# Kernel tuning notes

Hardware: AMD Instinct MI355X
Metric: run time of the kernel (lower is better)

## Reference

```python
import jax, jax.numpy as jnp
import numpy as np

B, D, U = 256, 2048, 2048  # batch, input_dim, units
EPS = 1e-8


def setup_inputs() -> dict:
    key = jax.random.key(0)
    ks = jax.random.split(key, 20)
    sd = 1.0 / np.sqrt(D)
    su = 1.0 / np.sqrt(U)
    inp = {
        'x': jax.random.normal(ks[0], (B, D), jnp.float32),
        'h_prev': jax.random.normal(ks[1], (B, U), jnp.float32),
        'c_prev': jax.random.normal(ks[2], (B, U), jnp.float32),
        'n_prev': jax.random.uniform(ks[3], (B, U), jnp.float32),
        'm_prev': jax.random.normal(ks[4], (B, U), jnp.float32),
        # input-to-gate weights (Dense with bias), keras layout [in, out]
        'Wz': jax.random.normal(ks[5], (D, U), jnp.float32) * sd,
        'Wi': jax.random.normal(ks[6], (D, U), jnp.float32) * sd,
        'Wf': jax.random.normal(ks[7], (D, U), jnp.float32) * sd,
        'Wo': jax.random.normal(ks[8], (D, U), jnp.float32) * sd,
        'bz': jnp.zeros((U,), jnp.float32),
        'bi': jnp.zeros((U,), jnp.float32),
        'bf': jnp.zeros((U,), jnp.float32),
        'bo': jnp.zeros((U,), jnp.float32),
        # recurrent weights (Dense without bias)
        'Uz': jax.random.normal(ks[9], (U, U), jnp.float32) * su,
        'Ui': jax.random.normal(ks[10], (U, U), jnp.float32) * su,
        'Uf': jax.random.normal(ks[11], (U, U), jnp.float32) * su,
        'Uo': jax.random.normal(ks[12], (U, U), jnp.float32) * su,
    }
    return inp


def reference(x, h_prev, c_prev, n_prev, m_prev,
              Wz, Wi, Wf, Wo, bz, bi, bf, bo, Uz, Ui, Uf, Uo):
    # fuse the 8 small GEMMs into 2 wide GEMMs (same math, gates split after)
    W = jnp.concatenate([Wz, Wi, Wf, Wo], axis=1)      # [D, 4U]
    Uc = jnp.concatenate([Uz, Ui, Uf, Uo], axis=1)     # [U, 4U]
    b = jnp.concatenate([bz, bi, bf, bo], axis=0)      # [4U]
    pre = x @ W + h_prev @ Uc + b                      # [B, 4U]
    z_tilde, i_tilde, f_tilde, o_tilde = jnp.split(pre, 4, axis=1)

    # exponential-gate stabilization (forget_gate_type='exponential')
    m_t = jnp.maximum(i_tilde + m_prev, i_tilde)
    i_t = jnp.exp(i_tilde - m_t)
    f_t = jnp.exp(f_tilde + m_prev - m_t)

    o_t = jax.nn.sigmoid(o_tilde)
    z_t = jnp.tanh(z_tilde)

    c_t = f_t * c_prev + i_t * z_t
    n_t = f_t * n_prev + i_t
    h_t = o_t * (c_t / (n_t + EPS))
    return jnp.stack([h_t, c_t, n_t, m_t], axis=0)  # [4, B, U]
```

## Files before the change

kernel.cpp:

```cpp
#include <hip/hip_runtime.h>
#include <cstdint>
#include <cstddef>

#define B_   256
#define D_   2048
#define U_   2048
#define NTOT 8192
#define BN   32
#define BK   64
#define KC   2048
#define ITERS (KC / BK)

typedef _Float16 half8 __attribute__((ext_vector_type(8)));
typedef float floatx16 __attribute__((ext_vector_type(16)));

__global__ __launch_bounds__(256) void prep_kernel(
    const float* __restrict__ x, const float* __restrict__ h,
    _Float16* __restrict__ Ahi)
{
    int gid   = blockIdx.x * 256 + threadIdx.x;
    int chunk = gid >> 8;
    int row   = gid & 255;
    int col0  = chunk * 8;
    const float* src = (col0 < D_) ? (x + row * D_ + col0)
                                   : (h + row * U_ + (col0 - D_));
    float4 v0 = *(const float4*)(src);
    float4 v1 = *(const float4*)(src + 4);
    float v[8] = {v0.x, v0.y, v0.z, v0.w, v1.x, v1.y, v1.z, v1.w};
    half8 hi;
#pragma unroll
    for (int i = 0; i < 8; ++i) hi[i] = (_Float16)v[i];
    *(half8*)(Ahi + (chunk * 256 + row) * 8) = hi;
}

__global__ __launch_bounds__(256) void gemm_kernel(
    const _Float16* __restrict__ Ahi,
    const float* __restrict__ Wz, const float* __restrict__ Wi,
    const float* __restrict__ Wf, const float* __restrict__ Wo,
    const float* __restrict__ Uz, const float* __restrict__ Ui,
    const float* __restrict__ Uf, const float* __restrict__ Uo,
    float* __restrict__ P)
{
    __shared__ __align__(16) _Float16 sA[2][8 * 256 * 8];
    __shared__ __align__(16) float    sB[2][BK * BN];

    const int t    = threadIdx.x;
    const int w    = t >> 6;
    const int lane = t & 63;
    const int lg   = lane >> 5;
    const int lm   = lane & 31;

    const int nblk = blockIdx.x;
    const int ks   = blockIdx.y;
    const int n0   = nblk * BN;
    const int g    = n0 >> 11;
    const int c0   = n0 & (U_ - 1);

    const float* wsel[8] = {Wz, Wi, Wf, Wo, Uz, Ui, Uf, Uo};
    const float* Bm = wsel[ks * 4 + g];
    const int chunk0 = ks * 256;

    const int arow_t = t;
    const int bk_t   = t >> 3;
    const int bc_t   = (t & 7) * 4;

    floatx16 acc[2] = {};

#define STAGE(kk, buf)                                                        \
    {                                                                         \
        int gch = chunk0 + (kk) * 8;                                          \
        _Pragma("unroll")                                                     \
        for (int i = 0; i < 8; ++i) {                                         \
            int gidx = ((gch + i) * 256 + arow_t) * 8;                        \
            int lidx = (i * 256 + arow_t) * 8;                                \
            __builtin_amdgcn_global_load_lds(                                 \
                (const __attribute__((address_space(1))) void*)(Ahi + gidx),  \
                (__attribute__((address_space(3))) void*)(&sA[buf][lidx]),    \
                16, 0, 0);                                                    \
        }                                                                     \
        _Pragma("unroll")                                                     \
        for (int j = 0; j < 2; ++j) {                                         \
            int krow = j * 32 + bk_t;                                         \
            const float* src = Bm + (size_t)((kk) * BK + krow) * U_ + c0 + bc_t; \
            __builtin_amdgcn_global_load_lds(                                 \
                (const __attribute__((address_space(1))) void*)(src),         \
                (__attribute__((address_space(3))) void*)(&sB[buf][krow * BN + bc_t]), \
                16, 0, 0);                                                    \
        }                                                                     \
    }

    STAGE(0, 0);
    __syncthreads();

    for (int kk = 0; kk < ITERS; ++kk) {
        int cur = kk & 1;
        if (kk + 1 < ITERS) STAGE(kk + 1, cur ^ 1);

#pragma unroll
        for (int kin = 0; kin < 4; ++kin) {
            half8 a0, a1, bf;
            {
                int chunkIdx = kin * 2 + lg;
                int row0 = w * 64 + lm;
                a0 = *(const half8*)(&sA[cur][(chunkIdx * 256 + row0) * 8]);
                a1 = *(const half8*)(&sA[cur][(chunkIdx * 256 + row0 + 32) * 8]);
            }
#pragma unroll
            for (int j = 0; j < 8; ++j) {
                float v = sB[cur][(kin * 16 + lg * 8 + j) * BN + lm];
                bf[j] = (_Float16)v;
            }
            acc[0] = __builtin_amdgcn_mfma_f32_32x32x16_f16(a0, bf, acc[0], 0, 0, 0);
            acc[1] = __builtin_amdgcn_mfma_f32_32x32x16_f16(a1, bf, acc[1], 0, 0, 0);
        }
        __syncthreads();
    }
#undef STAGE

    float* Pks = P + (size_t)ks * ((size_t)B_ * NTOT);
#pragma unroll
    for (int mt = 0; mt < 2; ++mt)
#pragma unroll
        for (int r = 0; r < 16; ++r) {
            int m = w * 64 + mt * 32 + 4 * lg + (r & 3) + 8 * (r >> 2);
            Pks[(size_t)m * NTOT + n0 + lm] = acc[mt][r];
        }
}

__global__ __launch_bounds__(256) void gates_kernel(
    const float* __restrict__ P,
    const float* __restrict__ c_prev, const float* __restrict__ n_prev,
    const float* __restrict__ m_prev,
    const float* __restrict__ bz, const float* __restrict__ bi,
    const float* __restrict__ bf, const float* __restrict__ bo,
    float* __restrict__ out)
{
    const size_t PS = (size_t)B_ * NTOT;
    const int OS = B_ * U_;
    int gid = blockIdx.x * 256 + threadIdx.x;
    int m = gid >> 9;
    int u = (gid & 511) * 4;

    float pre[4][4];
#pragma unroll
    for (int gi = 0; gi < 4; ++gi) {
        const float* base = P + (size_t)m * NTOT + gi * U_ + u;
        float4 s0 = *(const float4*)(base);
        float4 s1 = *(const float4*)(base + PS);
        pre[gi][0] = s0.x + s1.x;
        pre[gi][1] = s0.y + s1.y;
        pre[gi][2] = s0.z + s1.z;
        pre[gi][3] = s0.w + s1.w;
    }
    float4 bzv = *(const float4*)(bz + u);
    float4 biv = *(const float4*)(bi + u);
    float4 bfv = *(const float4*)(bf + u);
    float4 bov = *(const float4*)(bo + u);
    float bza[4] = {bzv.x, bzv.y, bzv.z, bzv.w};
    float bia[4] = {biv.x, biv.y, biv.z, biv.w};
    float bfa[4] = {bfv.x, bfv.y, bfv.z, bfv.w};
    float boa[4] = {bov.x, bov.y, bov.z, bov.w};

    float4 cp4 = *(const float4*)(c_prev + m * U_ + u);
    float4 np4 = *(const float4*)(n_prev + m * U_ + u);
    float4 mp4 = *(const float4*)(m_prev + m * U_ + u);
    float cpa[4] = {cp4.x, cp4.y, cp4.z, cp4.w};
    float npa[4] = {np4.x, np4.y, np4.z, np4.w};
    float mpa[4] = {mp4.x, mp4.y, mp4.z, mp4.w};

    float hr[4], cr[4], nr[4], mr[4];
#pragma unroll
    for (int e = 0; e < 4; ++e) {
        float zt = pre[0][e] + bza[e];
        float it = pre[1][e] + bia[e];
        float ft = pre[2][e] + bfa[e];
        float ot = pre[3][e] + boa[e];
        float mp = mpa[e];
        float m_t = fmaxf(it + mp, it);
        float i_t = expf(it - m_t);
        float f_t = expf(ft + mp - m_t);
        float o_t = 1.0f / (1.0f + expf(-ot));
        float z_t = tanhf(zt);
        float c_t = f_t * cpa[e] + i_t * z_t;
        float n_t = f_t * npa[e] + i_t;
        float h_t = o_t * (c_t / (n_t + 1e-8f));
        hr[e] = h_t; cr[e] = c_t; nr[e] = n_t; mr[e] = m_t;
    }
    float4 hv = {hr[0], hr[1], hr[2], hr[3]};
    float4 cv = {cr[0], cr[1], cr[2], cr[3]};
    float4 nv = {nr[0], nr[1], nr[2], nr[3]};
    float4 mv = {mr[0], mr[1], mr[2], mr[3]};
    *(float4*)(out + 0 * OS + m * U_ + u) = hv;
    *(float4*)(out + 1 * OS + m * U_ + u) = cv;
    *(float4*)(out + 2 * OS + m * U_ + u) = nv;
    *(float4*)(out + 3 * OS + m * U_ + u) = mv;
}

extern "C" void kernel_launch(void* const* d_in, const int* in_sizes, int n_in,
                              void* d_out, int out_size, void* d_ws, size_t ws_size,
                              hipStream_t stream)
{
    const float* x  = (const float*)d_in[0];
    const float* h  = (const float*)d_in[1];
    const float* cp = (const float*)d_in[2];
    const float* np = (const float*)d_in[3];
    const float* mp = (const float*)d_in[4];
    const float* Wz = (const float*)d_in[5];
    const float* Wi = (const float*)d_in[6];
    const float* Wf = (const float*)d_in[7];
    const float* Wo = (const float*)d_in[8];
    const float* bz = (const float*)d_in[9];
    const float* bi = (const float*)d_in[10];
    const float* bf = (const float*)d_in[11];
    const float* bo = (const float*)d_in[12];
    const float* Uz = (const float*)d_in[13];
    const float* Ui = (const float*)d_in[14];
    const float* Uf = (const float*)d_in[15];
    const float* Uo = (const float*)d_in[16];

    float* P = (float*)d_ws;
    _Float16* Ahi = (_Float16*)((char*)d_ws + (size_t)2 * B_ * NTOT * sizeof(float));

    prep_kernel<<<512, 256, 0, stream>>>(x, h, Ahi);
    gemm_kernel<<<dim3(256, 2), 256, 0, stream>>>(Ahi,
        Wz, Wi, Wf, Wo, Uz, Ui, Uf, Uo, P);
    gates_kernel<<<512, 256, 0, stream>>>(P, cp, np, mp, bz, bi, bf, bo,
        (float*)d_out);
}
```

Baseline: 210.7 us.

## Stream A operand from global, stage B as fp16 in padded LDS

```diff
diff --git a/kernel.cpp b/kernel.cpp
--- a/kernel.cpp
+++ b/kernel.cpp
@@ -2,14 +2,15 @@
 #include <cstdint>
 #include <cstddef>
 
-#define B_   256
-#define D_   2048
-#define U_   2048
-#define NTOT 8192
-#define BN   32
-#define BK   64
-#define KC   2048
-#define ITERS (KC / BK)
+#define B_    256
+#define D_    2048
+#define U_    2048
+#define NTOT  8192
+#define BN    32
+#define BK    128
+#define KSLICE 2048
+#define CHUNKS (KSLICE / BK)
+#define BPITCH 136
 
 typedef _Float16 half8 __attribute__((ext_vector_type(8)));
 typedef float floatx16 __attribute__((ext_vector_type(16)));
@@ -19,9 +20,9 @@
     _Float16* __restrict__ Ahi)
 {
     int gid   = blockIdx.x * 256 + threadIdx.x;
-    int chunk = gid >> 8;
+    int koct  = gid >> 8;
     int row   = gid & 255;
-    int col0  = chunk * 8;
+    int col0  = koct * 8;
     const float* src = (col0 < D_) ? (x + row * D_ + col0)
                                    : (h + row * U_ + (col0 - D_));
     float4 v0 = *(const float4*)(src);
@@ -30,7 +31,7 @@
     half8 hi;
 #pragma unroll
     for (int i = 0; i < 8; ++i) hi[i] = (_Float16)v[i];
-    *(half8*)(Ahi + (chunk * 256 + row) * 8) = hi;
+    *(half8*)(Ahi + (koct * 256 + row) * 8) = hi;
 }
 
 __global__ __launch_bounds__(256) void gemm_kernel(
@@ -41,8 +42,7 @@
     const float* __restrict__ Uf, const float* __restrict__ Uo,
     float* __restrict__ P)
 {
-    __shared__ __align__(16) _Float16 sA[2][8 * 256 * 8];
-    __shared__ __align__(16) float    sB[2][BK * BN];
+    __shared__ __align__(16) _Float16 sB[2][BN * BPITCH];
 
     const int t    = threadIdx.x;
     const int w    = t >> 6;
@@ -50,72 +50,68 @@
     const int lg   = lane >> 5;
     const int lm   = lane & 31;
 
-    const int nblk = blockIdx.x;
-    const int ks   = blockIdx.y;
-    const int n0   = nblk * BN;
-    const int g    = n0 >> 11;
-    const int c0   = n0 & (U_ - 1);
+    const int ntile = blockIdx.x;
+    const int ks    = blockIdx.y;
+    const int n0    = ntile * BN;
+    const int g     = n0 >> 11;
+    const int c0    = n0 & (U_ - 1);
+    const int koctB = ks * 256;
 
     const float* wsel[8] = {Wz, Wi, Wf, Wo, Uz, Ui, Uf, Uo};
-    const float* Bm = wsel[ks * 4 + g];
-    const int chunk0 = ks * 256;
-
-    const int arow_t = t;
-    const int bk_t   = t >> 3;
-    const int bc_t   = (t & 7) * 4;
+    const float* Bm   = wsel[ks * 4 + g];
+    const float* Bcol = Bm + c0 + lm;
+
+    const int bko = w * 2 + lg;
 
     floatx16 acc[2] = {};
-
-#define STAGE(kk, buf)                                                        \
+    float breg[2][8];
+
+#define LOAD_B(kk)                                                            \
     {                                                                         \
-        int gch = chunk0 + (kk) * 8;                                          \
-        _Pragma("unroll")                                                     \
-        for (int i = 0; i < 8; ++i) {                                         \
-            int gidx = ((gch + i) * 256 + arow_t) * 8;                        \
-            int lidx = (i * 256 + arow_t) * 8;                                \
-            __builtin_amdgcn_global_load_lds(                                 \
-                (const __attribute__((address_space(1))) void*)(Ahi + gidx),  \
-                (__attribute__((address_space(3))) void*)(&sA[buf][lidx]),    \
-                16, 0, 0);                                                    \
-        }                                                                     \
         _Pragma("unroll")                                                     \
         for (int j = 0; j < 2; ++j) {                                         \
-            int krow = j * 32 + bk_t;                                         \
-            const float* src = Bm + (size_t)((kk) * BK + krow) * U_ + c0 + bc_t; \
-            __builtin_amdgcn_global_load_lds(                                 \
-                (const __attribute__((address_space(1))) void*)(src),         \
-                (__attribute__((address_space(3))) void*)(&sB[buf][krow * BN + bc_t]), \
-                16, 0, 0);                                                    \
+            const float* src = Bcol + (size_t)((kk) * BK + (bko + 8 * j) * 8) * U_; \
+            _Pragma("unroll")                                                 \
+            for (int i = 0; i < 8; ++i)                                       \
+                breg[j][i] = src[(size_t)i * U_];                             \
         }                                                                     \
     }
 
-    STAGE(0, 0);
+#define WRITE_B(buf)                                                          \
+    {                                                                         \
+        _Pragma("unroll")                                                     \
+        for (int j = 0; j < 2; ++j) {                                         \
+            half8 hb;                                                         \
+            _Pragma("unroll")                                                 \
+            for (int i = 0; i < 8; ++i) hb[i] = (_Float16)breg[j][i];         \
+            *(half8*)(&sB[buf][lm * BPITCH + (bko + 8 * j) * 8]) = hb;        \
+        }                                                                     \
+    }
+
+    LOAD_B(0);
+    WRITE_B(0);
     __syncthreads();
 
-    for (int kk = 0; kk < ITERS; ++kk) {
+    const int arow0 = w * 64 + lm;
+
+    for (int kk = 0; kk < CHUNKS; ++kk) {
         int cur = kk & 1;
-        if (kk + 1 < ITERS) STAGE(kk + 1, cur ^ 1);
-
-#pragma unroll
-        for (int kin = 0; kin < 4; ++kin) {
-            half8 a0, a1, bf;
-            {
-                int chunkIdx = kin * 2 + lg;
-                int row0 = w * 64 + lm;
-                a0 = *(const half8*)(&sA[cur][(chunkIdx * 256 + row0) * 8]);
-                a1 = *(const half8*)(&sA[cur][(chunkIdx * 256 + row0 + 32) * 8]);
-            }
-#pragma unroll
-            for (int j = 0; j < 8; ++j) {
-                float v = sB[cur][(kin * 16 + lg * 8 + j) * BN + lm];
-                bf[j] = (_Float16)v;
-            }
-            acc[0] = __builtin_amdgcn_mfma_f32_32x32x16_f16(a0, bf, acc[0], 0, 0, 0);
-            acc[1] = __builtin_amdgcn_mfma_f32_32x32x16_f16(a1, bf, acc[1], 0, 0, 0);
+        if (kk + 1 < CHUNKS) LOAD_B(kk + 1);
+
+#pragma unroll
+        for (int kstep = 0; kstep < 8; ++kstep) {
+            int ko = koctB + kk * 16 + kstep * 2 + lg;
+            half8 a0 = *(const half8*)(Ahi + ((size_t)ko * 256 + arow0) * 8);
+            half8 a1 = *(const half8*)(Ahi + ((size_t)ko * 256 + arow0 + 32) * 8);
+            half8 b  = *(const half8*)(&sB[cur][lm * BPITCH + kstep * 16 + lg * 8]);
+            acc[0] = __builtin_amdgcn_mfma_f32_32x32x16_f16(a0, b, acc[0], 0, 0, 0);
+            acc[1] = __builtin_amdgcn_mfma_f32_32x32x16_f16(a1, b, acc[1], 0, 0, 0);
         }
+        if (kk + 1 < CHUNKS) WRITE_B(cur ^ 1);
         __syncthreads();
     }
-#undef STAGE
+#undef LOAD_B
+#undef WRITE_B
 
     float* Pks = P + (size_t)ks * ((size_t)B_ * NTOT);
 #pragma unroll
```

Result: slower. 218.5 us (+3.7%).
